# Kernel optimization log

Hardware: AMD Instinct MI355X
Metric: run time of the kernel (lower is better)

Reference implementation:

```python
import jax, jax.numpy as jnp
import numpy as np

N_NODES, N_EDGES, N_FEAT, DIM, HEADS, N_PRED, N_CLASS, N_STEPS = 10000, 160000, 64, 64, 4, 2, 16, 4


def setup_inputs() -> dict:
    key = jax.random.key(0)
    ks = jax.random.split(key, 16)
    def lin(k, fi, fo):
        return jax.random.normal(k, (fi, fo), jnp.float32) / np.sqrt(fi)
    return {
        "x": jax.random.normal(ks[0], (N_NODES, N_FEAT), jnp.float32),
        "edge_index": jax.random.randint(ks[1], (2, N_EDGES), 0, N_NODES, jnp.int64),
        "enc_W": lin(ks[2], N_FEAT, DIM), "enc_b": jnp.zeros((DIM,), jnp.float32),
        "gat_Wl": lin(ks[3], DIM, HEADS * DIM), "gat_bl": jnp.zeros((HEADS * DIM,), jnp.float32),
        "gat_Wr": lin(ks[4], DIM, HEADS * DIM), "gat_br": jnp.zeros((HEADS * DIM,), jnp.float32),
        "gat_att": jax.random.normal(ks[5], (HEADS, DIM), jnp.float32) / np.sqrt(DIM),
        "gat_bias": jnp.zeros((HEADS * DIM,), jnp.float32),
        "W1": lin(ks[6], HEADS * DIM, DIM), "b1": jnp.zeros((DIM,), jnp.float32),
        "W2": lin(ks[7], DIM, DIM), "b2": jnp.zeros((DIM,), jnp.float32),
        "act_W": lin(ks[8], DIM, 1), "act_b": jnp.zeros((1,), jnp.float32),
        "dec_W": jax.random.normal(ks[9], (N_PRED, DIM, N_CLASS), jnp.float32) / np.sqrt(DIM),
        "dec_b": jnp.zeros((N_PRED, N_CLASS), jnp.float32),
        "num_steps": N_STEPS,
    }


def reference(x, edge_index, enc_W, enc_b, gat_Wl, gat_bl, gat_Wr, gat_br,
              gat_att, gat_bias, W1, b1, W2, b2, act_W, act_b, dec_W, dec_b, num_steps):
    N = x.shape[0]
    H, C = gat_att.shape  # heads, per-head channels
    # PyG GATv2Conv adds self-loops by default
    loops = jnp.arange(N, dtype=edge_index.dtype)
    src = jnp.concatenate([edge_index[0], loops])
    dst = jnp.concatenate([edge_index[1], loops])

    h0 = x @ enc_W + enc_b  # encoder

    def step(carry, _):
        h, total, final = carry
        # GATv2: per-edge score on lin_l(src) + lin_r(dst)
        xl = (h @ gat_Wl + gat_bl).reshape(N, H, C)
        xr = (h @ gat_Wr + gat_br).reshape(N, H, C)
        e = jax.nn.leaky_relu(xl[src] + xr[dst], 0.2)          # [E, H, C]
        logits = jnp.einsum('ehc,hc->eh', e, gat_att)           # [E, H]
        m = jax.ops.segment_max(logits, dst, num_segments=N)    # segment softmax over dst
        ex = jnp.exp(logits - m[dst])
        denom = jax.ops.segment_sum(ex, dst, num_segments=N)
        alpha = ex / (denom[dst] + 1e-16)
        agg = jax.ops.segment_sum(xl[src] * alpha[:, :, None], dst, num_segments=N)
        g = agg.reshape(N, H * C) + gat_bias                    # concat heads + bias
        hn = jax.nn.relu(g @ W1 + b1) @ W2 + b2                 # process2 MLP
        # ACT halting: weighted accumulation, deltas clipped so weights sum to <= 1
        term = jax.nn.sigmoid(hn @ act_W + act_b)               # [N, 1]
        new_total = jnp.minimum(total + term, 1.0)
        delta = jnp.minimum(term, new_total - total)
        return (hn, total + delta, final + delta * hn), None

    carry0 = (h0, jnp.zeros((N, 1), x.dtype), jnp.zeros((N, h0.shape[1]), x.dtype))
    (_, _, final), _ = jax.lax.scan(step, carry0, None, length=num_steps)

    logits = jnp.einsum('nd,pdc->pnc', final, dec_W) + dec_b[:, None, :]
    return jax.nn.log_softmax(logits, axis=-1)  # [num_predictions, N, num_classes]
```

## Files before the change

kernel.cpp:

```cpp
#include <hip/hip_runtime.h>
#include <hip/hip_bf16.h>
#include <hip/hip_fp16.h>

#define N_NODES 10000
#define N_EDGES 160000
#define N_E2    (N_EDGES + N_NODES)
#define DIM     64
#define HD      256
#define N_PRED  2
#define N_CLASS 16
#define N_STEPS 4
#define BUCKET  64

typedef __hip_bfloat16 bf16;
__device__ __forceinline__ float b2f(bf16 v) { return __bfloat162float(v); }
__device__ __forceinline__ int clampn(int v) { return v < 0 ? 0 : (v >= N_NODES ? N_NODES - 1 : v); }

typedef _Float16 h2_t __attribute__((ext_vector_type(2)));

__device__ __forceinline__ float dot2(unsigned int a, unsigned int b, float c) {
#if __has_builtin(__builtin_amdgcn_fdot2)
    h2_t av, bv;
    __builtin_memcpy(&av, &a, 4);
    __builtin_memcpy(&bv, &b, 4);
    return __builtin_amdgcn_fdot2(av, bv, c, false);
#else
    __half2 ah = *(__half2*)&a, bh = *(__half2*)&b;
    float2 af = __half22float2(ah), bf = __half22float2(bh);
    return c + af.x * bf.x + af.y * bf.y;
#endif
}

struct ConvTable {
    const void* src[17];
    int start[18];
};

__device__ __forceinline__ float loadf(const void* p, int idx, int isbf16) {
    return isbf16 ? b2f(((const bf16*)p)[idx]) : ((const float*)p)[idx];
}

__global__ void detect_kernel(const unsigned int* __restrict__ e32,
                              const unsigned short* __restrict__ x16,
                              int* __restrict__ flags, int* __restrict__ cursor) {
    int i = blockIdx.x * 256 + threadIdx.x;
    if (i < N_NODES) cursor[i] = 0;
    if (blockIdx.x != 0) return;
    __shared__ int ce, cf;
    if (threadIdx.x == 0) { ce = 0; cf = 0; }
    __syncthreads();
    int le = 0;
    for (int k = threadIdx.x; k < 2048; k += 256)
        le += (e32[2 * k + 1] != 0u) ? 1 : 0;
    int lf = 0;
    for (int k = threadIdx.x; k < 1024; k += 256) {
        unsigned short u = x16[2 * k];
        int ex = (u >> 7) & 0xFF;
        lf += (u == 0 || (ex >= 114 && ex <= 141)) ? 1 : 0;
    }
    atomicAdd(&ce, le);
    atomicAdd(&cf, lf);
    __syncthreads();
    if (threadIdx.x == 0) {
        flags[0] = (ce < 1024) ? 1 : 0;
        flags[1] = (cf >= 512) ? 1 : 0;
    }
}

struct PreArgs {
    ConvTable tab;
    const void* Wl_raw; const void* Wr_raw; const void* W1_raw; const void* W2_raw;
    const int* edges;
    int cb, pb;
};

__global__ void pre_kernel(PreArgs a, const int* __restrict__ flags,
                           float* __restrict__ xf, __half* __restrict__ wp,
                           int* __restrict__ cursor, int* __restrict__ csr_src) {
    const int b = blockIdx.x, t = threadIdx.x;
    const int isb = flags[1];
    if (b < a.cb) {
        int i = b * 256 + t;
        if (i >= a.tab.start[17]) return;
        int j = 0;
        #pragma unroll
        for (int k = 1; k < 17; ++k) j += (i >= a.tab.start[k]) ? 1 : 0;
        xf[i] = loadf(a.tab.src[j], i - a.tab.start[j], isb);
    } else if (b < a.cb + a.pb) {
        int i = (b - a.cb) * 256 + t;
        if (i >= 26624) return;
        const void* base; int width, loc;
        if (i < 8192)       { loc = i;         base = a.Wl_raw; width = 256; }
        else if (i < 16384) { loc = i - 8192;  base = a.Wr_raw; width = 256; }
        else if (i < 24576) { loc = i - 16384; base = a.W1_raw; width = 64; }
        else                { loc = i - 24576; base = a.W2_raw; width = 64; }
        int k2 = loc / width, c = loc % width;
        wp[2 * i]     = __float2half(loadf(base, (2 * k2) * width + c, isb));
        wp[2 * i + 1] = __float2half(loadf(base, (2 * k2 + 1) * width + c, isb));
    } else {
        int e = (b - a.cb - a.pb) * 256 + t;
        if (e >= N_E2) return;
        int i64 = flags[0];
        int src, dst;
        if (e < N_EDGES) {
            src = clampn(i64 ? a.edges[2 * e] : a.edges[e]);
            dst = clampn(i64 ? a.edges[2 * (N_EDGES + e)] : a.edges[N_EDGES + e]);
        } else { src = dst = e - N_EDGES; }
        int pos = atomicAdd(&cursor[dst], 1);
        if (pos < BUCKET) csr_src[dst * BUCKET + pos] = src;
    }
}

__global__ __launch_bounds__(256) void enc_proj_kernel(
        const float* __restrict__ xf,
        int sX, int sEncW, int sEncB, int sWl, int sBl, int sWr, int sBr,
        __half* __restrict__ xlh, float* __restrict__ xr,
        float* __restrict__ act_tot, float* __restrict__ final_) {
    __shared__ float xs[8][DIM];
    __shared__ float h0[8][DIM];
    const int t = threadIdx.x, pp = t >> 6, d = t & 63;
    const int n0 = blockIdx.x * 8;
    const float* Xf   = xf + sX;
    const float* encW = xf + sEncW;
    const float* encB = xf + sEncB;
    const float* Wl   = xf + sWl;
    const float* bl   = xf + sBl;
    const float* Wr   = xf + sWr;
    const float* br   = xf + sBr;
    ((float*)xs)[t]       = Xf[n0 * DIM + t];
    ((float*)xs)[t + 256] = Xf[n0 * DIM + t + 256];
    final_[(size_t)n0 * DIM + t]       = 0.f;
    final_[(size_t)n0 * DIM + t + 256] = 0.f;
    if (t < 8) act_tot[n0 + t] = 0.f;
    __syncthreads();
    float ah0 = encB[d], ah1 = encB[d];
    for (int k = 0; k < DIM; ++k) {
        float wv = encW[k * DIM + d];
        ah0 += xs[pp][k] * wv;
        ah1 += xs[pp + 4][k] * wv;
    }
    h0[pp][d]     = ah0;
    h0[pp + 4][d] = ah1;
    __syncthreads();
    float al[8] = {0,0,0,0,0,0,0,0}, ar[8] = {0,0,0,0,0,0,0,0};
    for (int k = 0; k < DIM; ++k) {
        float wl = Wl[k * HD + t], wr = Wr[k * HD + t];
        #pragma unroll
        for (int j = 0; j < 8; ++j) { al[j] += h0[j][k] * wl; ar[j] += h0[j][k] * wr; }
    }
    float bbl = bl[t], bbr = br[t];
    #pragma unroll
    for (int j = 0; j < 8; ++j) {
        xlh[(size_t)(n0 + j) * HD + t] = __float2half(al[j] + bbl);
        xr[(size_t)(n0 + j) * HD + t] = ar[j] + bbr;
    }
}

__global__ __launch_bounds__(256) void step_kernel(
        const __half* __restrict__ xlh_in, const float* __restrict__ xr_in,
        const float* __restrict__ att, const float* __restrict__ gbias,
        const int* __restrict__ cursor, const int* __restrict__ csr_src,
        const __half* __restrict__ wp,
        const float* __restrict__ b1, const float* __restrict__ b2,
        const float* __restrict__ actW, const float* __restrict__ actB,
        const float* __restrict__ bl, const float* __restrict__ br,
        float* __restrict__ act_tot, float* __restrict__ final_,
        __half* __restrict__ xlh_out, float* __restrict__ xr_out, int do_proj) {
    __shared__ __align__(16) unsigned int gall_u[4][128];
    __shared__ float part[4][HD];
    __shared__ __half us_h[4][DIM];
    __shared__ float hns[4][DIM];
    __shared__ __half hns_h[4][DIM];
    __shared__ float delta[4];
    const int t = threadIdx.x, w = t >> 6, l = t & 63;
    const int pp = w, d = l;
    const int n0 = blockIdx.x * 4;
    const int n = n0 + w;

    {
        int deg = cursor[n]; deg = (deg > BUCKET) ? BUCKET : deg;
        const int e0 = n * BUCKET;
        const int e1 = e0 + deg;
        const int elast = e1 - 1;
        const float4 xr4 = ((const float4*)(xr_in + (size_t)n * HD))[l];
        const float4 at4 = ((const float4*)att)[l];
        float m = -1e30f, s = 0.f;
        float4 acc = {0.f, 0.f, 0.f, 0.f};
        uint2 A[4], B[4];
        #pragma unroll
        for (int i = 0; i < 4; ++i) {
            int ee = e0 + i; ee = (ee > elast) ? elast : ee;
            A[i] = ((const uint2*)(xlh_in + (size_t)csr_src[ee] * HD))[l];
        }
        for (int base = e0; base < e1; base += 4) {
            #pragma unroll
            for (int i = 0; i < 4; ++i) {
                int ee = base + 4 + i; ee = (ee > elast) ? elast : ee;
                B[i] = ((const uint2*)(xlh_in + (size_t)csr_src[ee] * HD))[l];
            }
            #pragma unroll
            for (int i = 0; i < 4; ++i) {
                const bool valid = (base + i) < e1;
                __half2 h01 = *reinterpret_cast<__half2*>(&A[i].x);
                __half2 h23 = *reinterpret_cast<__half2*>(&A[i].y);
                float2 f01 = __half22float2(h01);
                float2 f23 = __half22float2(h23);
                float c0 = f01.x, c1 = f01.y, c2 = f23.x, c3 = f23.y;
                float z0 = c0 + xr4.x, z1 = c1 + xr4.y, z2 = c2 + xr4.z, z3 = c3 + xr4.w;
                z0 = (z0 > 0.f) ? z0 : 0.2f * z0;
                z1 = (z1 > 0.f) ? z1 : 0.2f * z1;
                z2 = (z2 > 0.f) ? z2 : 0.2f * z2;
                z3 = (z3 > 0.f) ? z3 : 0.2f * z3;
                float p = z0 * at4.x + z1 * at4.y + z2 * at4.z + z3 * at4.w;
                #pragma unroll
                for (int mo = 8; mo; mo >>= 1) p += __shfl_xor(p, mo, 64);
                p = valid ? p : -1e30f;
                float nm = fmaxf(m, p);
                float sc = __expf(m - nm);
                float wv = __expf(p - nm);
                s = s * sc + wv;
                acc.x = acc.x * sc + wv * c0;
                acc.y = acc.y * sc + wv * c1;
                acc.z = acc.z * sc + wv * c2;
                acc.w = acc.w * sc + wv * c3;
                m = nm;
            }
            #pragma unroll
            for (int i = 0; i < 4; ++i) A[i] = B[i];
        }
        const float inv = 1.f / (s + 1e-16f);
        const float4 gb4 = ((const float4*)gbias)[l];
        __half2 o01 = __floats2half2_rn(acc.x * inv + gb4.x, acc.y * inv + gb4.y);
        __half2 o23 = __floats2half2_rn(acc.z * inv + gb4.z, acc.w * inv + gb4.w);
        uint2 outv2;
        outv2.x = *(unsigned int*)&o01;
        outv2.y = *(unsigned int*)&o23;
        ((uint2*)gall_u[w])[l] = outv2;
    }
    __syncthreads();

    const unsigned int* Wlp = (const unsigned int*)wp;
    const unsigned int* Wrp = Wlp + 8192;
    const unsigned int* W1p = Wlp + 16384;
    const unsigned int* W2p = Wlp + 24576;

    {
        float acc[4] = {0.f, 0.f, 0.f, 0.f};
        for (int k2 = pp * 32; k2 < pp * 32 + 32; ++k2) {
            unsigned int w2 = W1p[k2 * 64 + d];
            #pragma unroll
            for (int j = 0; j < 4; ++j) acc[j] = dot2(gall_u[j][k2], w2, acc[j]);
        }
        #pragma unroll
        for (int j = 0; j < 4; ++j) part[j][t] = acc[j];
    }
    __syncthreads();
    {
        float v = part[pp][d] + part[pp][64 + d] + part[pp][128 + d] + part[pp][192 + d] + b1[d];
        us_h[pp][d] = __float2half(fmaxf(v, 0.f));
    }
    __syncthreads();
    {
        const unsigned int* us_u = (const unsigned int*)us_h;
        float acc[4] = {0.f, 0.f, 0.f, 0.f};
        for (int k2 = pp * 8; k2 < pp * 8 + 8; ++k2) {
            unsigned int w2 = W2p[k2 * 64 + d];
            #pragma unroll
            for (int j = 0; j < 4; ++j) acc[j] = dot2(us_u[j * 32 + k2], w2, acc[j]);
        }
        #pragma unroll
        for (int j = 0; j < 4; ++j) part[j][t] = acc[j];
    }
    __syncthreads();
    {
        float hv = part[pp][d] + part[pp][64 + d] + part[pp][128 + d] + part[pp][192 + d] + b2[d];
        hns[pp][d] = hv;
        hns_h[pp][d] = __float2half(hv);
    }
    __syncthreads();
    {
        float p = hns[pp][d] * actW[d];
        #pragma unroll
        for (int mo = 32; mo; mo >>= 1) p += __shfl_xor(p, mo, 64);
        if (d == 0) {
            float term = 1.f / (1.f + __expf(-(p + actB[0])));
            float tot = act_tot[n0 + pp];
            float nt = fminf(tot + term, 1.f);
            float dl = fminf(term, nt - tot);
            act_tot[n0 + pp] = tot + dl;
            delta[pp] = dl;
        }
    }
    __syncthreads();
    final_[(size_t)(n0 + pp) * DIM + d] += delta[pp] * hns[pp][d];

    if (do_proj) {
        const unsigned int* hn_u = (const unsigned int*)hns_h;
        float al[4] = {0.f, 0.f, 0.f, 0.f}, ar[4] = {0.f, 0.f, 0.f, 0.f};
        for (int k2 = 0; k2 < 32; ++k2) {
            unsigned int wl2 = Wlp[k2 * 256 + t];
            unsigned int wr2 = Wrp[k2 * 256 + t];
            #pragma unroll
            for (int j = 0; j < 4; ++j) {
                unsigned int hh = hn_u[j * 32 + k2];
                al[j] = dot2(hh, wl2, al[j]);
                ar[j] = dot2(hh, wr2, ar[j]);
            }
        }
        float bbl = bl[t], bbr = br[t];
        #pragma unroll
        for (int j = 0; j < 4; ++j) {
            xlh_out[(size_t)(n0 + j) * HD + t] = __float2half(al[j] + bbl);
            xr_out[(size_t)(n0 + j) * HD + t] = ar[j] + bbr;
        }
    }
}

__global__ void decoder_kernel(const float* __restrict__ final_,
                               const float* __restrict__ decW, const float* __restrict__ decB,
                               const int* __restrict__ flags, void* __restrict__ outv) {
    int id = blockIdx.x * 256 + threadIdx.x;
    if (id >= N_NODES * N_PRED * N_CLASS) return;
    int n = id >> 5, r = id & 31, p = r >> 4, c = r & 15;
    float acc = decB[p * N_CLASS + c];
    for (int dd = 0; dd < DIM; ++dd)
        acc += final_[(size_t)n * DIM + dd] * decW[(p * DIM + dd) * N_CLASS + c];
    float mx = acc;
    #pragma unroll
    for (int mo = 8; mo; mo >>= 1) mx = fmaxf(mx, __shfl_xor(mx, mo, 64));
    float ex = __expf(acc - mx);
    float ss = ex;
    #pragma unroll
    for (int mo = 8; mo; mo >>= 1) ss += __shfl_xor(ss, mo, 64);
    float ov = acc - mx - logf(ss);
    int oi = p * (N_NODES * N_CLASS) + n * N_CLASS + c;
    if (flags[1]) ((bf16*)outv)[oi] = __float2bfloat16(ov);
    else          ((float*)outv)[oi] = ov;
}

static size_t align256(size_t x) { return (x + 255) & ~size_t(255); }

extern "C" void kernel_launch(void* const* d_in, const int* in_sizes, int n_in,
                              void* d_out, int out_size, void* d_ws, size_t ws_size,
                              hipStream_t stream) {
    const int* edges = (const int*)d_in[1];

    static const int fids[17] = {0, 2, 3, 4, 5, 6, 7, 8, 9, 10, 11, 12, 13, 14, 15, 16, 17};
    ConvTable tab;
    int cum = 0;
    for (int i = 0; i < 17; ++i) {
        tab.src[i] = d_in[fids[i]];
        tab.start[i] = cum;
        cum += in_sizes[fids[i]];
    }
    tab.start[17] = cum;

    char* w = (char*)d_ws;
    size_t o = 0;
    int* flags     = (int*)(w + o); o = align256(o + 16 * sizeof(int));
    int* cursor    = (int*)(w + o); o = align256(o + N_NODES * sizeof(int));
    float* act_tot = (float*)(w + o); o = align256(o + N_NODES * sizeof(float));
    float* final_  = (float*)(w + o); o = align256(o + (size_t)N_NODES * DIM * sizeof(float));
    int* csr_src   = (int*)(w + o); o = align256(o + (size_t)N_NODES * BUCKET * sizeof(int));
    float* xf      = (float*)(w + o); o = align256(o + (size_t)cum * sizeof(float));
    __half* xlh_a  = (__half*)(w + o); o = align256(o + (size_t)N_NODES * HD * sizeof(__half));
    float* xr_a    = (float*)(w + o); o = align256(o + (size_t)N_NODES * HD * sizeof(float));
    __half* xlh_b  = (__half*)(w + o); o = align256(o + (size_t)N_NODES * HD * sizeof(__half));
    float* xr_b    = (float*)(w + o); o = align256(o + (size_t)N_NODES * HD * sizeof(float));
    __half* wpack  = (__half*)(w + o); o = align256(o + 53248 * sizeof(__half));
    if (o > ws_size) return;

    const float* att  = xf + tab.start[7];
    const float* gbias= xf + tab.start[8];
    const float* b1   = xf + tab.start[10];
    const float* b2   = xf + tab.start[12];
    const float* actW = xf + tab.start[13];
    const float* actB = xf + tab.start[14];
    const float* decW = xf + tab.start[15];
    const float* decB = xf + tab.start[16];

    detect_kernel<<<(N_NODES + 255) / 256, 256, 0, stream>>>(
        (const unsigned int*)d_in[1], (const unsigned short*)d_in[0], flags, cursor);

    PreArgs pa;
    pa.tab = tab;
    pa.Wl_raw = d_in[4]; pa.Wr_raw = d_in[6]; pa.W1_raw = d_in[10]; pa.W2_raw = d_in[12];
    pa.edges = edges;
    pa.cb = (cum + 255) / 256;
    pa.pb = (26624 + 255) / 256;
    int sb = (N_E2 + 255) / 256;
    pre_kernel<<<pa.cb + pa.pb + sb, 256, 0, stream>>>(pa, flags, xf, wpack, cursor, csr_src);

    enc_proj_kernel<<<N_NODES / 8, 256, 0, stream>>>(
        xf, tab.start[0], tab.start[1], tab.start[2],
        tab.start[3], tab.start[4], tab.start[5], tab.start[6],
        xlh_a, xr_a, act_tot, final_);

    __half* xl_in = xlh_a;  float* xr_in = xr_a;
    __half* xl_out = xlh_b; float* xr_out = xr_b;
    for (int step = 0; step < N_STEPS; ++step) {
        step_kernel<<<N_NODES / 4, 256, 0, stream>>>(
            xl_in, xr_in, att, gbias, cursor, csr_src, wpack,
            b1, b2, actW, actB,
            xf + tab.start[4], xf + tab.start[6],
            act_tot, final_, xl_out, xr_out, (step < N_STEPS - 1) ? 1 : 0);
        __half* th = xl_in; xl_in = xl_out; xl_out = th;
        float* tf = xr_in; xr_in = xr_out; xr_out = tf;
    }

    int db = (N_NODES * N_PRED * N_CLASS + 255) / 256;
    decoder_kernel<<<db, 256, 0, stream>>>(final_, decW, decB, flags, d_out);
}
```

Measured before the change: 295.7 us.

## Sort nodes by in-degree so step blocks process similar-degree nodes

Adds a single-block counting-sort kernel that builds a permutation of nodes ordered by clamped in-degree, and makes each step_kernel block process four nodes taken from that permutation. Each wavefront handles one node, so grouping nodes of equal degree is meant to cut load imbalance inside a block, where the slowest wave delays the shared MLP phase. The cost is an extra serial single-block launch, an indirection through perm, and scattered writes of node outputs that no longer follow contiguous node order.

```diff
diff --git a/kernel.cpp b/kernel.cpp
--- a/kernel.cpp
+++ b/kernel.cpp
@@ -111,6 +111,31 @@
     }
 }
 
+__global__ void degsort_kernel(const int* __restrict__ cursor, int* __restrict__ perm) {
+    __shared__ int bins[BUCKET + 1];
+    __shared__ int offs[BUCKET + 1];
+    const int t = threadIdx.x;
+    if (t <= BUCKET) bins[t] = 0;
+    __syncthreads();
+    for (int n = t; n < N_NODES; n += 256) {
+        int d = cursor[n]; d = (d > BUCKET) ? BUCKET : d;
+        atomicAdd(&bins[d], 1);
+    }
+    __syncthreads();
+    if (t == 0) {
+        int s = 0;
+        for (int i = 0; i <= BUCKET; ++i) { offs[i] = s; s += bins[i]; }
+    }
+    __syncthreads();
+    if (t <= BUCKET) bins[t] = 0;
+    __syncthreads();
+    for (int n = t; n < N_NODES; n += 256) {
+        int d = cursor[n]; d = (d > BUCKET) ? BUCKET : d;
+        int p = offs[d] + atomicAdd(&bins[d], 1);
+        perm[p] = n;
+    }
+}
+
 __global__ __launch_bounds__(256) void enc_proj_kernel(
         const float* __restrict__ xf,
         int sX, int sEncW, int sEncB, int sWl, int sBl, int sWr, int sBr,
@@ -160,6 +185,7 @@
         const __half* __restrict__ xlh_in, const float* __restrict__ xr_in,
         const float* __restrict__ att, const float* __restrict__ gbias,
         const int* __restrict__ cursor, const int* __restrict__ csr_src,
+        const int* __restrict__ perm,
         const __half* __restrict__ wp,
         const float* __restrict__ b1, const float* __restrict__ b2,
         const float* __restrict__ actW, const float* __restrict__ actB,
@@ -175,7 +201,7 @@
     const int t = threadIdx.x, w = t >> 6, l = t & 63;
     const int pp = w, d = l;
     const int n0 = blockIdx.x * 4;
-    const int n = n0 + w;
+    const int n = perm[n0 + w];
 
     {
         int deg = cursor[n]; deg = (deg > BUCKET) ? BUCKET : deg;
@@ -284,15 +310,15 @@
         for (int mo = 32; mo; mo >>= 1) p += __shfl_xor(p, mo, 64);
         if (d == 0) {
             float term = 1.f / (1.f + __expf(-(p + actB[0])));
-            float tot = act_tot[n0 + pp];
+            float tot = act_tot[n];
             float nt = fminf(tot + term, 1.f);
             float dl = fminf(term, nt - tot);
-            act_tot[n0 + pp] = tot + dl;
+            act_tot[n] = tot + dl;
             delta[pp] = dl;
         }
     }
     __syncthreads();
-    final_[(size_t)(n0 + pp) * DIM + d] += delta[pp] * hns[pp][d];
+    final_[(size_t)n * DIM + d] += delta[pp] * hns[pp][d];
 
     if (do_proj) {
         const unsigned int* hn_u = (const unsigned int*)hns_h;
@@ -310,8 +336,9 @@
         float bbl = bl[t], bbr = br[t];
         #pragma unroll
         for (int j = 0; j < 4; ++j) {
-            xlh_out[(size_t)(n0 + j) * HD + t] = __float2half(al[j] + bbl);
-            xr_out[(size_t)(n0 + j) * HD + t] = ar[j] + bbr;
+            int nj = perm[n0 + j];
+            xlh_out[(size_t)nj * HD + t] = __float2half(al[j] + bbl);
+            xr_out[(size_t)nj * HD + t] = ar[j] + bbr;
         }
     }
 }
@@ -362,6 +389,7 @@
     float* act_tot = (float*)(w + o); o = align256(o + N_NODES * sizeof(float));
     float* final_  = (float*)(w + o); o = align256(o + (size_t)N_NODES * DIM * sizeof(float));
     int* csr_src   = (int*)(w + o); o = align256(o + (size_t)N_NODES * BUCKET * sizeof(int));
+    int* perm      = (int*)(w + o); o = align256(o + N_NODES * sizeof(int));
     float* xf      = (float*)(w + o); o = align256(o + (size_t)cum * sizeof(float));
     __half* xlh_a  = (__half*)(w + o); o = align256(o + (size_t)N_NODES * HD * sizeof(__half));
     float* xr_a    = (float*)(w + o); o = align256(o + (size_t)N_NODES * HD * sizeof(float));
@@ -391,6 +419,8 @@
     int sb = (N_E2 + 255) / 256;
     pre_kernel<<<pa.cb + pa.pb + sb, 256, 0, stream>>>(pa, flags, xf, wpack, cursor, csr_src);
 
+    degsort_kernel<<<1, 256, 0, stream>>>(cursor, perm);
+
     enc_proj_kernel<<<N_NODES / 8, 256, 0, stream>>>(
         xf, tab.start[0], tab.start[1], tab.start[2],
         tab.start[3], tab.start[4], tab.start[5], tab.start[6],
@@ -400,7 +430,7 @@
     __half* xl_out = xlh_b; float* xr_out = xr_b;
     for (int step = 0; step < N_STEPS; ++step) {
         step_kernel<<<N_NODES / 4, 256, 0, stream>>>(
-            xl_in, xr_in, att, gbias, cursor, csr_src, wpack,
+            xl_in, xr_in, att, gbias, cursor, csr_src, perm, wpack,
             b1, b2, actW, actB,
             xf + tab.start[4], xf + tab.start[6],
             act_tot, final_, xl_out, xr_out, (step < N_STEPS - 1) ? 1 : 0);
```

After: 315.4 us. 6.7% more time.
